# Kernel optimization log

Measured on AMD Instinct MI355X. Metric: run time of the kernel, lower is better.

## Reference

```python
import jax, jax.numpy as jnp
import numpy as np

NUM_EMBEDDINGS = 8192
EMBEDDING_DIM = 512
COMMITMENT_COST = 0.25


def setup_inputs() -> dict:
    key = jax.random.key(0)
    kz, ke = jax.random.split(key)
    z = jax.random.normal(kz, (2, EMBEDDING_DIM, 8, 32, 32), dtype=jnp.float32)
    # matches nn.Embedding init uniform_(-1/K, 1/K)
    emb_w = jax.random.uniform(
        ke, (NUM_EMBEDDINGS, EMBEDDING_DIM), dtype=jnp.float32,
        minval=-1.0 / NUM_EMBEDDINGS, maxval=1.0 / NUM_EMBEDDINGS)
    return {"z": z, "emb_w": emb_w}


def reference(z, emb_w):
    B, C, F, H, W = z.shape
    # [B,C,F,H,W] -> [N, C]
    z_flat = jnp.transpose(z, (0, 2, 3, 4, 1)).reshape(-1, C)
    # squared L2 distances via expansion: |z|^2 + |e|^2 - 2 z.e
    dist = (jnp.sum(z_flat * z_flat, axis=1, keepdims=True)
            + jnp.sum(emb_w * emb_w, axis=1)
            - 2.0 * jnp.matmul(z_flat, emb_w.T))  # [N, K]
    indices = jnp.argmin(dist, axis=1)  # [N]
    z_q_flat = emb_w[indices]  # [N, C]
    z_q = jnp.transpose(z_q_flat.reshape(B, F, H, W, C), (0, 4, 1, 2, 3))
    diff = z_q - z
    mse = jnp.mean(diff * diff)
    # codebook_loss == commitment_loss numerically (detach only affects grads)
    vq_loss = mse + COMMITMENT_COST * mse
    # straight-through estimator: value equals z_q
    z_q_ste = z + jax.lax.stop_gradient(z_q - z)
    indices = indices.reshape(B, F, H, W)
    return (z_q_ste, vq_loss, indices)
```

## Files before the change

### kernel.cpp

```cpp
#include <hip/hip_runtime.h>


constexpr int KCB = 8192;
constexpr int CD  = 512;
constexpr int SD  = 8192;
constexpr int NB  = 2;
constexpr int NR  = NB * SD;
constexpr long ZQ_ELEMS = (long)NB * CD * SD;

constexpr size_t WS_CNT   = 64;
constexpr size_t WS_KEYS  = 128;
constexpr size_t WS_RISK  = 139264;
constexpr size_t WS_IDX   = 212992;
constexpr size_t WS_LIST  = 286720;
constexpr size_t WS_ZNORM = 360448;
constexpr size_t WS_ENORM = 425984;
constexpr size_t WS_EMBT  = 458752;
constexpr size_t WS_ZH    = 17235968;
constexpr size_t WS_ZM    = 34013184;
constexpr size_t WS_EH    = 50790400;
constexpr size_t WS_EM    = 59179008;

#define RISK_EPS 2.0e-7f
#define WINDOW   1.3e-4f

constexpr int BUFB = 50176;

typedef __attribute__((ext_vector_type(8))) short short8;
typedef __attribute__((ext_vector_type(4))) float f32x4;

__device__ __forceinline__ unsigned int fkey(float f) {
  unsigned int b = __float_as_uint(f);
  return (b & 0x80000000u) ? ~b : (b | 0x80000000u);
}
__device__ __forceinline__ float unfkey(unsigned int u) {
  return (u & 0x80000000u) ? __uint_as_float(u ^ 0x80000000u)
                           : __uint_as_float(~u);
}
__device__ __forceinline__ ushort bf16_rne(float f, float* back) {
  unsigned int u = __float_as_uint(f);
  ushort h = (ushort)((u + 0x7FFFu + ((u >> 16) & 1u)) >> 16);
  *back = __uint_as_float((unsigned int)h << 16);
  return h;
}
__device__ __forceinline__ void gload16(const void* g, void* l) {
  __builtin_amdgcn_global_load_lds(
      (const __attribute__((address_space(1))) unsigned int*)g,
      (__attribute__((address_space(3))) unsigned int*)l, 16, 0, 0);
}

__global__ __launch_bounds__(256) void k_znorm(const float* __restrict__ z,
                                               float* __restrict__ znorm) {
  int n0 = blockIdx.x * 256;
  int b = n0 / SD, s0 = n0 % SD;
  const float* zp = z + (size_t)b * CD * SD + s0 + threadIdx.x;
  double a = 0.0;
  #pragma unroll 8
  for (int c = 0; c < CD; ++c) {
    double v = (double)zp[(size_t)c * SD];
    a = fma(v, v, a);
  }
  znorm[n0 + threadIdx.x] = (float)a;
}

__global__ __launch_bounds__(256) void k_enorm(const float* __restrict__ emb,
                                               float* __restrict__ enorm) {
  int row  = blockIdx.x * 4 + (threadIdx.x >> 6);
  int lane = threadIdx.x & 63;
  const float4* p = (const float4*)(emb + (size_t)row * CD);
  float4 a = p[lane * 2], b = p[lane * 2 + 1];
  float s = a.x*a.x + a.y*a.y + a.z*a.z + a.w*a.w
          + b.x*b.x + b.y*b.y + b.z*b.z + b.w*b.w;
  #pragma unroll
  for (int off = 32; off; off >>= 1) s += __shfl_down(s, off);
  if (lane == 0) enorm[row] = s;
}

__global__ __launch_bounds__(256) void k_transpose(const float* __restrict__ emb,
                                                   float* __restrict__ embt) {
  __shared__ float t[64][65];
  int bk = blockIdx.x & 127, bc = blockIdx.x >> 7;
  int k0 = bk * 64, c0 = bc * 64;
  int t4 = threadIdx.x & 15, tq = threadIdx.x >> 4;
  #pragma unroll
  for (int p = 0; p < 4; ++p) {
    int kk = p * 16 + tq;
    float4 v = *(const float4*)(emb + (size_t)(k0 + kk) * CD + c0 + 4 * t4);
    t[kk][4*t4+0] = v.x; t[kk][4*t4+1] = v.y; t[kk][4*t4+2] = v.z; t[kk][4*t4+3] = v.w;
  }
  __syncthreads();
  #pragma unroll
  for (int p = 0; p < 4; ++p) {
    int cc = p * 16 + tq;
    float4 v;
    v.x = t[4*t4+0][cc]; v.y = t[4*t4+1][cc]; v.z = t[4*t4+2][cc]; v.w = t[4*t4+3][cc];
    *(float4*)(embt + (size_t)(c0 + cc) * KCB + k0 + 4 * t4) = v;
  }
}


__global__ __launch_bounds__(256) void k_zsplit(const float* __restrict__ z,
                                                ushort* __restrict__ zh,
                                                ushort* __restrict__ zm) {
  __shared__ float t[32][257];
  int rt = blockIdx.x >> 4, ct = blockIdx.x & 15;
  int n0 = rt * 256;
  int b = n0 >> 13, s0 = n0 & (SD - 1);
  const float* zp = z + (size_t)b * CD * SD + (size_t)(ct * 32) * SD + s0;
  #pragma unroll 4
  for (int c = 0; c < 32; ++c)
    t[c][threadIdx.x] = zp[(size_t)c * SD + threadIdx.x];
  __syncthreads();
  size_t tbase = ((size_t)rt * 16 + ct) * 8192;
  #pragma unroll
  for (int p = 0; p < 4; ++p) {
    int slot = p * 256 + threadIdx.x;
    int r = slot >> 2, cs = slot & 3;
    int csw = cs ^ ((r >> 1) & 3);
    union { ushort u[8]; int4 v; } ph, pm;
    #pragma unroll
    for (int j = 0; j < 8; ++j) {
      float f = t[cs * 8 + j][r];
      float fh, fm;
      ph.u[j] = bf16_rne(f, &fh);
      float r1 = f - fh;
      pm.u[j] = bf16_rne(r1, &fm);
    }
    size_t off = tbase + (size_t)r * 32 + csw * 8;
    *(int4*)(zh + off) = ph.v;
    *(int4*)(zm + off) = pm.v;
  }
}

__global__ __launch_bounds__(256) void k_esplit(const float* __restrict__ emb,
                                                ushort* __restrict__ eh,
                                                ushort* __restrict__ em) {
  __shared__ float t[32][257];
  int rt = blockIdx.x >> 4, ct = blockIdx.x & 15;
  int k0 = rt * 256;
  #pragma unroll 4
  for (int i = 0; i < 32; ++i) {
    int idx = i * 256 + threadIdx.x;
    int r = idx >> 5, c = idx & 31;
    t[c][r] = emb[(size_t)(k0 + r) * CD + ct * 32 + c];
  }
  __syncthreads();
  size_t tbase = ((size_t)rt * 16 + ct) * 8192;
  #pragma unroll
  for (int p = 0; p < 4; ++p) {
    int slot = p * 256 + threadIdx.x;
    int r = slot >> 2, cs = slot & 3;
    int csw = cs ^ ((r >> 1) & 3);
    union { ushort u[8]; int4 v; } ph, pm;
    #pragma unroll
    for (int j = 0; j < 8; ++j) {
      float f = t[cs * 8 + j][r];
      float fh, fm;
      ph.u[j] = bf16_rne(f, &fh);
      float r1 = f - fh;
      pm.u[j] = bf16_rne(r1, &fm);
    }
    size_t off = tbase + (size_t)r * 32 + csw * 8;
    *(int4*)(eh + off) = ph.v;
    *(int4*)(em + off) = pm.v;
  }
}

__global__ __launch_bounds__(512, 2) void k_dist_mfma(
    const ushort* __restrict__ zh, const ushort* __restrict__ zm,
    const ushort* __restrict__ eh, const ushort* __restrict__ em,
    const float* __restrict__ enorm_g, const float* __restrict__ znorm,
    unsigned long long* __restrict__ keys, unsigned int* __restrict__ riskArr) {
  extern __shared__ __align__(16) char smem[];

  int tid  = threadIdx.x;
  int lane = tid & 63;
  int wid  = tid >> 6;
  int wm = wid >> 2, wn = wid & 3;
  int lk = lane >> 4, lc = lane & 15;

  int bid = (int)blockIdx.x;
  int swz = (bid & 7) * 32 + (bid >> 3);
  int m0    = (swz >> 1) * 128;
  int khalf = swz & 1;
  int n_rt  = m0 >> 8;
  int ahalf = (m0 >> 7) & 1;

  size_t thr8  = (size_t)tid * 8;
  int    tid16 = tid * 16;
  int    lane16 = lane * 16;

  int afo[4], bfo[4];
  #pragma unroll
  for (int mi = 0; mi < 4; ++mi) {
    int rowA = wm * 64 + mi * 16 + lc;
    afo[mi] = rowA * 64 + ((lk ^ ((rowA >> 1) & 3)) << 4);
  }
  #pragma unroll
  for (int ni = 0; ni < 4; ++ni) {
    int rowB = wn * 64 + ni * 16 + lc;
    bfo[ni] = rowB * 64 + ((lk ^ ((rowB >> 1) & 3)) << 4);
  }

  float Aab[16];
  #pragma unroll
  for (int li = 0; li < 16; ++li)
    Aab[li] = znorm[m0 + wm * 64 + (li >> 2) * 16 + lk * 4 + (li & 3)];

  unsigned long long bkey[16];
  float rminv[16];
  #pragma unroll
  for (int li = 0; li < 16; ++li) { bkey[li] = ~0ull; rminv[li] = 3.402823466e38f; }

#define STAGE(s_) do {                                                   \
    int it_ = (s_) >> 4, ks_ = (s_) & 15;                                \
    char* lb_ = smem + ((s_) % 3) * BUFB;                                \
    size_t ae_ = (size_t)(n_rt * 16 + ks_) * 8192 + (size_t)ahalf * 4096 \
                 + thr8;                                                 \
    size_t be_ = (size_t)((khalf * 16 + it_) * 16 + ks_) * 8192 + thr8;  \
    gload16(zh + ae_,        lb_ + tid16);                               \
    gload16(zm + ae_,        lb_ + 8192 + tid16);                        \
    gload16(eh + be_,        lb_ + 16384 + tid16);                       \
    gload16(eh + be_ + 4096, lb_ + 24576 + tid16);                       \
    gload16(em + be_,        lb_ + 32768 + tid16);                       \
    gload16(em + be_ + 4096, lb_ + 40960 + tid16);                       \
    gload16(enorm_g + (size_t)(khalf * 4096 + it_ * 256) + lane * 4,     \
            lb_ + 49152 + lane16);                                       \
  } while (0)

  STAGE(0);
  STAGE(1);

  for (int it = 0; it < 16; ++it) {
    f32x4 acc[4][4];
    #pragma unroll
    for (int mi = 0; mi < 4; ++mi)
      #pragma unroll
      for (int ni = 0; ni < 4; ++ni) {
        f32x4 zz = {0.f, 0.f, 0.f, 0.f};
        acc[mi][ni] = zz;
      }

    for (int ks = 0; ks < 16; ++ks) {
      int s = it * 16 + ks;
      if (s + 2 < 256) asm volatile("s_waitcnt vmcnt(7)" ::: "memory");
      else             asm volatile("s_waitcnt vmcnt(0)" ::: "memory");
      __builtin_amdgcn_s_barrier();
      __builtin_amdgcn_sched_barrier(0);
      if (s + 2 < 256) STAGE(s + 2);

      const char* Cb = smem + (s % 3) * BUFB;
      short8 a_h[4], a_m[4];
      #pragma unroll
      for (int mi = 0; mi < 4; ++mi) {
        a_h[mi] = *(const short8*)(Cb + afo[mi]);
        a_m[mi] = *(const short8*)(Cb + 8192 + afo[mi]);
      }
      #pragma unroll
      for (int ni = 0; ni < 4; ++ni) {
        short8 b_h = *(const short8*)(Cb + 16384 + bfo[ni]);
        short8 b_m = *(const short8*)(Cb + 32768 + bfo[ni]);
        #pragma unroll
        for (int mi = 0; mi < 4; ++mi)
          acc[mi][ni] = __builtin_amdgcn_mfma_f32_16x16x32_bf16(a_h[mi], b_h, acc[mi][ni], 0, 0, 0);
        #pragma unroll
        for (int mi = 0; mi < 4; ++mi)
          acc[mi][ni] = __builtin_amdgcn_mfma_f32_16x16x32_bf16(a_h[mi], b_m, acc[mi][ni], 0, 0, 0);
        #pragma unroll
        for (int mi = 0; mi < 4; ++mi)
          acc[mi][ni] = __builtin_amdgcn_mfma_f32_16x16x32_bf16(a_m[mi], b_h, acc[mi][ni], 0, 0, 0);
        #pragma unroll
        for (int mi = 0; mi < 4; ++mi)
          acc[mi][ni] = __builtin_amdgcn_mfma_f32_16x16x32_bf16(a_m[mi], b_m, acc[mi][ni], 0, 0, 0);
      }
    }

    int N0 = khalf * 4096 + it * 256;
    const char* Eb = smem + ((it * 16 + 15) % 3) * BUFB + 49152;
    #pragma unroll
    for (int ni = 0; ni < 4; ++ni) {
      int coff = wn * 64 + ni * 16 + lc;
      int col = N0 + coff;
      float en = *(const float*)(Eb + coff * 4);
      #pragma unroll
      for (int mi = 0; mi < 4; ++mi) {
        #pragma unroll
        for (int r = 0; r < 4; ++r) {
          int li = mi * 4 + r;
          float ab = Aab[li] + en;
          float q  = -2.0f * acc[mi][ni][r];
          float sv = ab + q;
          float bvv = sv - ab;
          float t   = q - bvv;
          unsigned int su = __float_as_uint(sv);
          float ulp = __uint_as_float(su & 0x7f800000u) * 1.1920929e-7f;
          bool risky = (0.5f * ulp - fabsf(t)) < RISK_EPS;
          if (((su & 0x7fffffu) == 0u) && (t < 0.f))
            risky |= ((0.25f * ulp + t) < RISK_EPS);
          unsigned long long key =
              ((unsigned long long)fkey(sv) << 32) | (unsigned int)col;
          if (key < bkey[li]) bkey[li] = key;
          if (risky && sv < rminv[li]) rminv[li] = sv;
        }
      }
    }
  }
#undef STAGE

  __syncthreads();
  unsigned long long* red = (unsigned long long*)smem;
  #pragma unroll
  for (int li = 0; li < 16; ++li) {
    int row = wm * 64 + (li >> 2) * 16 + lk * 4 + (li & 3);
    red[row * 64 + wn * 16 + lc] = bkey[li];
  }
  __syncthreads();
  if (tid < 128) {
    unsigned long long mn = ~0ull;
    #pragma unroll 4
    for (int i = 0; i < 64; ++i) {
      unsigned long long v = red[tid * 64 + i];
      if (v < mn) mn = v;
    }
    atomicMin(&keys[m0 + tid], mn);
  }
  __syncthreads();
  unsigned int* red2 = (unsigned int*)smem;
  #pragma unroll
  for (int li = 0; li < 16; ++li) {
    int row = wm * 64 + (li >> 2) * 16 + lk * 4 + (li & 3);
    red2[row * 64 + wn * 16 + lc] = fkey(rminv[li]);
  }
  __syncthreads();
  if (tid < 128) {
    unsigned int mn = 0xFFFFFFFFu;
    #pragma unroll 4
    for (int i = 0; i < 64; ++i) {
      unsigned int v = red2[tid * 64 + i];
      if (v < mn) mn = v;
    }
    atomicMin(&riskArr[m0 + tid], mn);
  }
}

__global__ __launch_bounds__(256) void k_resolve(const unsigned long long* __restrict__ keys,
                                                 const unsigned int* __restrict__ riskArr,
                                                 int* __restrict__ idxArr,
                                                 int* __restrict__ list,
                                                 unsigned int* __restrict__ cnt) {
  int row = blockIdx.x * 256 + threadIdx.x;
  unsigned long long kk = keys[row];
  idxArr[row] = (int)(kk & 0xffffffffull) & (KCB - 1);
  float smin = unfkey((unsigned int)(kk >> 32));
  float rmin = unfkey(riskArr[row]);
  if (rmin <= smin + WINDOW) {
    unsigned int pos = atomicAdd(cnt, 1u);
    list[pos & (NR - 1)] = row;
  }
}

__global__ __launch_bounds__(256) void k_rescan(const float* __restrict__ z,
                                                const float* __restrict__ embt,
                                                const float* __restrict__ enorm,
                                                const float* __restrict__ znorm,
                                                const int* __restrict__ list,
                                                const unsigned int* __restrict__ cnt,
                                                int* __restrict__ idxArr) {
  __shared__ float zs[512];
  __shared__ unsigned long long rk[256];
  int tid = threadIdx.x;
  unsigned int nr = *cnt;
  if (nr > (unsigned int)NR) nr = NR;
  for (unsigned int li = blockIdx.x; li < nr; li += gridDim.x) {
    int row = list[li] & (NR - 1);
    int b = row >> 13, s = row & (SD - 1);
    const float* zp = z + (size_t)b * CD * SD + s;
    zs[tid]       = zp[(size_t)tid * SD];
    zs[tid + 256] = zp[(size_t)(tid + 256) * SD];
    __syncthreads();
    float A = znorm[row];
    unsigned long long best = ~0ull;
    #pragma unroll 1
    for (int g = 0; g < 8; ++g) {
      int ka = tid + g * 1024;
      float a0 = 0.f, a1 = 0.f, a2 = 0.f, a3 = 0.f;
      #pragma unroll 8
      for (int c = 0; c < CD; ++c) {
        const float* ep = embt + (size_t)c * KCB + ka;
        float zc = zs[c];
        a0 = fmaf(zc, ep[0],   a0);
        a1 = fmaf(zc, ep[256], a1);
        a2 = fmaf(zc, ep[512], a2);
        a3 = fmaf(zc, ep[768], a3);
      }
      float av[4] = {a0, a1, a2, a3};
      #pragma unroll
      for (int jj = 0; jj < 4; ++jj) {
        int k = ka + jj * 256;
        float d = (A + enorm[k]) - 2.0f * av[jj];
        unsigned long long key =
            ((unsigned long long)fkey(d) << 32) | (unsigned int)k;
        if (key < best) best = key;
      }
    }
    rk[tid] = best;
    __syncthreads();
    for (int s2 = 128; s2; s2 >>= 1) {
      if (tid < s2 && rk[tid + s2] < rk[tid]) rk[tid] = rk[tid + s2];
      __syncthreads();
    }
    if (tid == 0) idxArr[row] = (int)(rk[0] & 0xffffffffull) & (KCB - 1);
    __syncthreads();
  }
}

__global__ __launch_bounds__(256) void k_gather(const float* __restrict__ z,
                                                const float* __restrict__ emb,
                                                const int* __restrict__ idxArr,
                                                float* __restrict__ out,
                                                double* __restrict__ acc) {
  __shared__ float q[16][516];
  __shared__ int   idxs[16];
  __shared__ float wpart[4];
  int tid = threadIdx.x;
  int n0 = blockIdx.x * 16;
  int b = n0 / SD, s0 = n0 % SD;
  if (tid < 16) {
    int idx = idxArr[n0 + tid] & (KCB - 1);
    idxs[tid] = idx;
    out[ZQ_ELEMS + 1 + n0 + tid] = (float)idx;
  }
  __syncthreads();
  int row = tid >> 4, c4 = (tid & 15) * 4;
  const float* esrc = emb + (size_t)idxs[row] * CD;
  #pragma unroll
  for (int p = 0; p < 8; ++p) {
    int c = c4 + p * 64;
    *(float4*)&q[row][c] = *(const float4*)(esrc + c);
  }
  __syncthreads();
  int si = tid & 15, cq = tid >> 4;
  float sum = 0.f;
  const float* zrd = z   + (size_t)b * CD * SD + s0 + si;
  float*       owr = out + (size_t)b * CD * SD + s0 + si;
  #pragma unroll
  for (int j = 0; j < 32; ++j) {
    int c = cq + 16 * j;
    float zv = zrd[(size_t)c * SD];
    float qv = q[si][c];
    float d = qv - zv;
    sum += d * d;
    owr[(size_t)c * SD] = zv + (qv - zv);
  }
  #pragma unroll
  for (int off = 32; off; off >>= 1) sum += __shfl_down(sum, off);
  if ((tid & 63) == 0) wpart[tid >> 6] = sum;
  __syncthreads();
  if (tid == 0) {
    double t = (double)wpart[0] + (double)wpart[1] + (double)wpart[2] + (double)wpart[3];
    atomicAdd(acc, t);
  }
}

__global__ void k_loss(const double* __restrict__ acc, float* __restrict__ out) {
  out[ZQ_ELEMS] = (float)(1.25 * (*acc) / (double)ZQ_ELEMS);
}

extern "C" void kernel_launch(void* const* d_in, const int* in_sizes, int n_in,
                              void* d_out, int out_size, void* d_ws, size_t ws_size,
                              hipStream_t stream) {
  const float* z   = (const float*)d_in[0];
  const float* emb = (const float*)d_in[1];
  float* out = (float*)d_out;
  double*             acc   = (double*)d_ws;
  unsigned int*       cnt   = (unsigned int*)((char*)d_ws + WS_CNT);
  unsigned long long* keys  = (unsigned long long*)((char*)d_ws + WS_KEYS);
  unsigned int*       risk  = (unsigned int*)((char*)d_ws + WS_RISK);
  int*                idxA  = (int*)((char*)d_ws + WS_IDX);
  int*                list  = (int*)((char*)d_ws + WS_LIST);
  float*              znorm = (float*)((char*)d_ws + WS_ZNORM);
  float*              enorm = (float*)((char*)d_ws + WS_ENORM);
  float*              embt  = (float*)((char*)d_ws + WS_EMBT);
  ushort* zh = (ushort*)((char*)d_ws + WS_ZH);
  ushort* zm = (ushort*)((char*)d_ws + WS_ZM);
  ushort* eh = (ushort*)((char*)d_ws + WS_EH);
  ushort* em = (ushort*)((char*)d_ws + WS_EM);
  (void)in_sizes; (void)n_in; (void)out_size; (void)ws_size;

  hipMemsetAsync(d_ws, 0, 128, stream);
  hipMemsetAsync((char*)d_ws + WS_KEYS, 0xFF, (size_t)NR * 8, stream);
  hipMemsetAsync((char*)d_ws + WS_RISK, 0xFF, (size_t)NR * 4, stream);

  k_znorm    <<<NR / 256, 256, 0, stream>>>(z, znorm);
  k_enorm    <<<KCB / 4, 256, 0, stream>>>(emb, enorm);
  k_transpose<<<(KCB / 64) * (CD / 64), 256, 0, stream>>>(emb, embt);
  k_zsplit   <<<(NR / 256) * 16, 256, 0, stream>>>(z, zh, zm);
  k_esplit   <<<(KCB / 256) * 16, 256, 0, stream>>>(emb, eh, em);
  k_dist_mfma<<<256, 512, 3 * BUFB, stream>>>(zh, zm, eh, em,
                                              enorm, znorm, keys, risk);
  k_resolve  <<<NR / 256, 256, 0, stream>>>(keys, risk, idxA, list, cnt);
  k_rescan   <<<256, 256, 0, stream>>>(z, embt, enorm, znorm, list, cnt, idxA);
  k_gather   <<<NR / 16, 256, 0, stream>>>(z, emb, idxA, out, acc);
  k_loss     <<<1, 1, 0, stream>>>(acc, out);
}
```

Baseline: 753.6 us.

## Double-buffer B fragments in registers and raise priority around MFMA clusters

Restructures the GEMM inner loop into pairs of k-steps. During each step, the B fragments for the next step are read from shared memory into alternating register sets, overlapping those LDS reads with the current MFMA cluster. The MFMA block is wrapped in s_setprio to favour matrix issue. In exchange, every step now waits with vmcnt(0) instead of vmcnt(7), so global prefetch depth effectively drops to one stage, and the extra register buffers raise register pressure.

After: 852.6 us. +13.1%, slower.

```diff
diff --git a/kernel.cpp b/kernel.cpp
--- a/kernel.cpp
+++ b/kernel.cpp
@@ -228,8 +228,57 @@
             lb_ + 49152 + lane16);                                       \
   } while (0)
 
+#define READ_B(s_, BH, BM) do {                                          \
+    const char* Rb_ = smem + ((s_) % 3) * BUFB;                          \
+    _Pragma("unroll")                                                    \
+    for (int ni_ = 0; ni_ < 4; ++ni_) {                                  \
+      BH[ni_] = *(const short8*)(Rb_ + 16384 + bfo[ni_]);                \
+      BM[ni_] = *(const short8*)(Rb_ + 32768 + bfo[ni_]);                \
+    }                                                                    \
+  } while (0)
+
+#define CLUSTER(s_, BH, BM) do {                                         \
+    const char* Cb_ = smem + ((s_) % 3) * BUFB;                          \
+    short8 a_h[4], a_m[4];                                               \
+    _Pragma("unroll")                                                    \
+    for (int mi_ = 0; mi_ < 4; ++mi_) {                                  \
+      a_h[mi_] = *(const short8*)(Cb_ + afo[mi_]);                       \
+      a_m[mi_] = *(const short8*)(Cb_ + 8192 + afo[mi_]);                \
+    }                                                                    \
+    __builtin_amdgcn_sched_barrier(0);                                   \
+    __builtin_amdgcn_s_setprio(1);                                       \
+    _Pragma("unroll")                                                    \
+    for (int ni_ = 0; ni_ < 4; ++ni_) {                                  \
+      _Pragma("unroll")                                                  \
+      for (int mi_ = 0; mi_ < 4; ++mi_)                                  \
+        acc[mi_][ni_] = __builtin_amdgcn_mfma_f32_16x16x32_bf16(a_h[mi_], BH[ni_], acc[mi_][ni_], 0, 0, 0); \
+      _Pragma("unroll")                                                  \
+      for (int mi_ = 0; mi_ < 4; ++mi_)                                  \
+        acc[mi_][ni_] = __builtin_amdgcn_mfma_f32_16x16x32_bf16(a_h[mi_], BM[ni_], acc[mi_][ni_], 0, 0, 0); \
+      _Pragma("unroll")                                                  \
+      for (int mi_ = 0; mi_ < 4; ++mi_)                                  \
+        acc[mi_][ni_] = __builtin_amdgcn_mfma_f32_16x16x32_bf16(a_m[mi_], BH[ni_], acc[mi_][ni_], 0, 0, 0); \
+      _Pragma("unroll")                                                  \
+      for (int mi_ = 0; mi_ < 4; ++mi_)                                  \
+        acc[mi_][ni_] = __builtin_amdgcn_mfma_f32_16x16x32_bf16(a_m[mi_], BM[ni_], acc[mi_][ni_], 0, 0, 0); \
+    }                                                                    \
+    __builtin_amdgcn_s_setprio(0);                                       \
+  } while (0)
+
+#define SYNC_STEP() do {                                                 \
+    asm volatile("s_waitcnt vmcnt(0)" ::: "memory");                     \
+    __builtin_amdgcn_s_barrier();                                        \
+    __builtin_amdgcn_sched_barrier(0);                                   \
+  } while (0)
+
+  short8 bhE[4], bmE[4], bhO[4], bmO[4];
+
   STAGE(0);
   STAGE(1);
+  asm volatile("s_waitcnt vmcnt(7)" ::: "memory");
+  __builtin_amdgcn_s_barrier();
+  __builtin_amdgcn_sched_barrier(0);
+  READ_B(0, bhE, bmE);
 
   for (int it = 0; it < 16; ++it) {
     f32x4 acc[4][4];
@@ -241,38 +290,17 @@
         acc[mi][ni] = zz;
       }
 
-    for (int ks = 0; ks < 16; ++ks) {
-      int s = it * 16 + ks;
-      if (s + 2 < 256) asm volatile("s_waitcnt vmcnt(7)" ::: "memory");
-      else             asm volatile("s_waitcnt vmcnt(0)" ::: "memory");
-      __builtin_amdgcn_s_barrier();
-      __builtin_amdgcn_sched_barrier(0);
-      if (s + 2 < 256) STAGE(s + 2);
-
-      const char* Cb = smem + (s % 3) * BUFB;
-      short8 a_h[4], a_m[4];
-      #pragma unroll
-      for (int mi = 0; mi < 4; ++mi) {
-        a_h[mi] = *(const short8*)(Cb + afo[mi]);
-        a_m[mi] = *(const short8*)(Cb + 8192 + afo[mi]);
-      }
-      #pragma unroll
-      for (int ni = 0; ni < 4; ++ni) {
-        short8 b_h = *(const short8*)(Cb + 16384 + bfo[ni]);
-        short8 b_m = *(const short8*)(Cb + 32768 + bfo[ni]);
-        #pragma unroll
-        for (int mi = 0; mi < 4; ++mi)
-          acc[mi][ni] = __builtin_amdgcn_mfma_f32_16x16x32_bf16(a_h[mi], b_h, acc[mi][ni], 0, 0, 0);
-        #pragma unroll
-        for (int mi = 0; mi < 4; ++mi)
-          acc[mi][ni] = __builtin_amdgcn_mfma_f32_16x16x32_bf16(a_h[mi], b_m, acc[mi][ni], 0, 0, 0);
-        #pragma unroll
-        for (int mi = 0; mi < 4; ++mi)
-          acc[mi][ni] = __builtin_amdgcn_mfma_f32_16x16x32_bf16(a_m[mi], b_h, acc[mi][ni], 0, 0, 0);
-        #pragma unroll
-        for (int mi = 0; mi < 4; ++mi)
-          acc[mi][ni] = __builtin_amdgcn_mfma_f32_16x16x32_bf16(a_m[mi], b_m, acc[mi][ni], 0, 0, 0);
-      }
+    #pragma unroll
+    for (int kp = 0; kp < 8; ++kp) {
+      int x0 = it * 16 + kp * 2;
+      SYNC_STEP();
+      if (x0 + 2 < 256) STAGE(x0 + 2);
+      if (x0 + 1 < 256) READ_B(x0 + 1, bhO, bmO);
+      CLUSTER(x0, bhE, bmE);
+      SYNC_STEP();
+      if (x0 + 3 < 256) STAGE(x0 + 3);
+      if (x0 + 2 < 256) READ_B(x0 + 2, bhE, bmE);
+      CLUSTER(x0 + 1, bhO, bmO);
     }
 
     int N0 = khalf * 4096 + it * 256;
@@ -305,6 +333,9 @@
       }
     }
   }
+#undef SYNC_STEP
+#undef CLUSTER
+#undef READ_B
 #undef STAGE
 
   __syncthreads();
```

## Drop low-low bf16 split product in distance MFMA and widen gather tiles

Applied to the files above, without the earlier changes.

Removes the a_m*b_m term from the bf16x3 split-precision distance matmul, cutting the MFMA work in the main distance kernel by a quarter. This slightly lowers the accuracy of the approximate distances, and the existing risk window and rescan step are relied on to catch near-ties. The gather kernel is also restructured to handle 64 rows per block, staging codebook rows in 128-channel chunks so that z reads and output writes are coalesced 64-wide along the spatial axis.

Measured after the change: 685.9 us. 1.1x faster.

```diff
diff --git a/kernel.cpp b/kernel.cpp
--- a/kernel.cpp
+++ b/kernel.cpp
@@ -269,9 +269,6 @@
         #pragma unroll
         for (int mi = 0; mi < 4; ++mi)
           acc[mi][ni] = __builtin_amdgcn_mfma_f32_16x16x32_bf16(a_m[mi], b_h, acc[mi][ni], 0, 0, 0);
-        #pragma unroll
-        for (int mi = 0; mi < 4; ++mi)
-          acc[mi][ni] = __builtin_amdgcn_mfma_f32_16x16x32_bf16(a_m[mi], b_m, acc[mi][ni], 0, 0, 0);
       }
     }
 
@@ -419,38 +416,46 @@
                                                 const int* __restrict__ idxArr,
                                                 float* __restrict__ out,
                                                 double* __restrict__ acc) {
-  __shared__ float q[16][516];
-  __shared__ int   idxs[16];
+  __shared__ float q[64][129];
+  __shared__ int   idxs[64];
   __shared__ float wpart[4];
   int tid = threadIdx.x;
-  int n0 = blockIdx.x * 16;
-  int b = n0 / SD, s0 = n0 % SD;
-  if (tid < 16) {
+  int n0 = blockIdx.x * 64;
+  int b = n0 >> 13, s0 = n0 & (SD - 1);
+  if (tid < 64) {
     int idx = idxArr[n0 + tid] & (KCB - 1);
     idxs[tid] = idx;
     out[ZQ_ELEMS + 1 + n0 + tid] = (float)idx;
   }
   __syncthreads();
-  int row = tid >> 4, c4 = (tid & 15) * 4;
-  const float* esrc = emb + (size_t)idxs[row] * CD;
-  #pragma unroll
-  for (int p = 0; p < 8; ++p) {
-    int c = c4 + p * 64;
-    *(float4*)&q[row][c] = *(const float4*)(esrc + c);
-  }
-  __syncthreads();
-  int si = tid & 15, cq = tid >> 4;
+  int sl = tid & 63;
+  int cg = tid >> 6;
   float sum = 0.f;
-  const float* zrd = z   + (size_t)b * CD * SD + s0 + si;
-  float*       owr = out + (size_t)b * CD * SD + s0 + si;
-  #pragma unroll
-  for (int j = 0; j < 32; ++j) {
-    int c = cq + 16 * j;
-    float zv = zrd[(size_t)c * SD];
-    float qv = q[si][c];
-    float d = qv - zv;
-    sum += d * d;
-    owr[(size_t)c * SD] = zv + (qv - zv);
+  const float* zb = z   + (size_t)b * CD * SD + s0 + sl;
+  float*       ob = out + (size_t)b * CD * SD + s0 + sl;
+  for (int cc = 0; cc < 4; ++cc) {
+    int cbase = cc * 128;
+    __syncthreads();
+    {
+      int r = tid >> 2, p = tid & 3;
+      const float* e = emb + (size_t)idxs[r] * CD + cbase + p * 32;
+      #pragma unroll
+      for (int j = 0; j < 8; ++j) {
+        float4 v = *(const float4*)(e + j * 4);
+        q[r][p*32 + j*4 + 0] = v.x; q[r][p*32 + j*4 + 1] = v.y;
+        q[r][p*32 + j*4 + 2] = v.z; q[r][p*32 + j*4 + 3] = v.w;
+      }
+    }
+    __syncthreads();
+    #pragma unroll 8
+    for (int j = 0; j < 32; ++j) {
+      int c = cbase + cg * 32 + j;
+      float zv = zb[(size_t)c * SD];
+      float qv = q[sl][cg * 32 + j];
+      float d = qv - zv;
+      sum += d * d;
+      ob[(size_t)c * SD] = zv + (qv - zv);
+    }
   }
   #pragma unroll
   for (int off = 32; off; off >>= 1) sum += __shfl_down(sum, off);
@@ -500,6 +505,6 @@
                                               enorm, znorm, keys, risk);
   k_resolve  <<<NR / 256, 256, 0, stream>>>(keys, risk, idxA, list, cnt);
   k_rescan   <<<256, 256, 0, stream>>>(z, embt, enorm, znorm, list, cnt, idxA);
-  k_gather   <<<NR / 16, 256, 0, stream>>>(z, emb, idxA, out, acc);
+  k_gather   <<<NR / 64, 256, 0, stream>>>(z, emb, idxA, out, acc);
   k_loss     <<<1, 1, 0, stream>>>(acc, out);
 }
```
